# Performance work log

Hardware: AMD Instinct MI355X
Metric: run time of the kernel (lower is better)

Reference implementation:

```python
import jax, jax.numpy as jnp
import numpy as np

B, L, D = 8, 4096, 256
G, K = 64, 16
N = G * K  # 1024 slots


def _gelu(x):
    return jax.nn.gelu(x, approximate=False)  # torch nn.GELU default = exact erf


def setup_inputs() -> dict:
    key = jax.random.key(0)
    ks = jax.random.split(key, 12)
    r = lambda k, shp, s: jax.random.normal(k, shp, jnp.float32) * s
    d = D
    return {
        "X": r(ks[0], (B, L, d), 1.0),
        "S": r(ks[1], (B, N, d), 1.0),
        # projections stored (in, out); torch Linear is x @ W.T + b
        "Wgroup": r(ks[2], (d, G), d ** -0.5),
        "Wslot": r(ks[3], (d, K), d ** -0.5),
        "Wm1": r(ks[4], (d, 2 * d), d ** -0.5), "bm1": jnp.zeros((2 * d,), jnp.float32),
        "Wm2": r(ks[5], (2 * d, d), (2 * d) ** -0.5), "bm2": jnp.zeros((d,), jnp.float32),
        "Wg1": r(ks[6], (d, d), d ** -0.5), "bg1": jnp.zeros((d,), jnp.float32),
        "Wg2": r(ks[7], (d, 1), d ** -0.5), "bg2": jnp.zeros((1,), jnp.float32),
        "Wu1": r(ks[8], (2 * d, 2 * d), (2 * d) ** -0.5), "bu1": jnp.zeros((2 * d,), jnp.float32),
        "Wu2": r(ks[9], (2 * d, d), (2 * d) ** -0.5), "bu2": jnp.zeros((d,), jnp.float32),
        "ln_w": jnp.ones((d,), jnp.float32), "ln_b": jnp.zeros((d,), jnp.float32),
    }


def reference(X, S, Wgroup, Wslot, Wm1, bm1, Wm2, bm2, Wg1, bg1, Wg2, bg2,
              Wu1, bu1, Wu2, bu2, ln_w, ln_b):
    # message + gate per token
    msg = _gelu(X @ Wm1 + bm1) @ Wm2 + bm2                  # (B,L,D)
    gate = jax.nn.sigmoid(_gelu(X @ Wg1 + bg1) @ Wg2 + bg2)  # (B,L,1)
    gated_msg = msg * gate                                   # (B,L,D)

    # eval-mode hierarchical WTA: hard argmax one-hot routing (group, then slot)
    group_idx = jnp.argmax(X @ Wgroup, axis=-1)              # (B,L) in [0,G)
    slot_idx = jnp.argmax(X @ Wslot, axis=-1)                # (B,L) in [0,K)
    flat_slot = group_idx * K + slot_idx                     # (B,L) in [0,N)

    # one-hot bmm == scatter-sum of gated messages into slots (exact same math)
    seg = (flat_slot + jnp.arange(B)[:, None] * N).reshape(-1)  # (B*L,)
    incoming = jax.ops.segment_sum(gated_msg.reshape(B * L, D), seg,
                                   num_segments=B * N).reshape(B, N, D)

    # slot update + LayerNorm
    h = jnp.concatenate([S, incoming], axis=-1)              # (B,N,2D)
    S_new = S + (_gelu(h @ Wu1 + bu1) @ Wu2 + bu2)
    mu = S_new.mean(-1, keepdims=True)
    var = S_new.var(-1, keepdims=True)
    return (S_new - mu) * jax.lax.rsqrt(var + 1e-5) * ln_w + ln_b
```

## Files before the change

### kernel.cpp

```cpp
#include <hip/hip_runtime.h>
#include <hip/hip_bf16.h>

using bf16 = __hip_bfloat16;
typedef __attribute__((ext_vector_type(8))) __bf16 bf16x8;
typedef __attribute__((ext_vector_type(4))) float f32x4;

namespace {

constexpr int D     = 256;
constexpr int NTOK  = 32768;
constexpr int NSLOT = 8192;
constexpr int GG    = 64;
constexpr int KK    = 16;
constexpr int NN    = 1024;

__device__ __forceinline__ float erf_fast(float x){
  const float ax = fabsf(x);
  const float tt = 1.0f / fmaf(0.3275911f, ax, 1.0f);
  float p = fmaf(1.061405429f, tt, -1.453152027f);
  p = fmaf(p, tt, 1.421413741f);
  p = fmaf(p, tt, -0.284496736f);
  p = fmaf(p, tt, 0.254829592f);
  p *= tt;
  const float e = __expf(-ax*ax);
  const float r = 1.0f - p*e;
  return copysignf(r, x);
}

__device__ __forceinline__ float gelu_f(float x){
  return 0.5f * x * (1.0f + erf_fast(x * 0.70710678118654752f));
}

struct alignas(16) ushort8s { unsigned short v[8]; };

__device__ __forceinline__ ushort8s pack8(const float* src){
  const float4 f0 = reinterpret_cast<const float4*>(src)[0];
  const float4 f1 = reinterpret_cast<const float4*>(src)[1];
  ushort8s u;
  u.v[0] = __bfloat16_as_ushort(__float2bfloat16(f0.x));
  u.v[1] = __bfloat16_as_ushort(__float2bfloat16(f0.y));
  u.v[2] = __bfloat16_as_ushort(__float2bfloat16(f0.z));
  u.v[3] = __bfloat16_as_ushort(__float2bfloat16(f0.w));
  u.v[4] = __bfloat16_as_ushort(__float2bfloat16(f1.x));
  u.v[5] = __bfloat16_as_ushort(__float2bfloat16(f1.y));
  u.v[6] = __bfloat16_as_ushort(__float2bfloat16(f1.z));
  u.v[7] = __bfloat16_as_ushort(__float2bfloat16(f1.w));
  return u;
}


__global__ void prep_w_k(const float* __restrict__ Wm1, const float* __restrict__ Wg1,
                         const float* __restrict__ Wm2, const float* __restrict__ Wu1,
                         const float* __restrict__ Wu2, const float* __restrict__ Wgr,
                         const float* __restrict__ Wsl, const float* __restrict__ bm1,
                         const float* __restrict__ bg1,
                         bf16* __restrict__ W1p, bf16* __restrict__ W2p,
                         bf16* __restrict__ Wu1p, bf16* __restrict__ Wu2p,
                         float* __restrict__ Wcat, float* __restrict__ bcat)
{
  const int idx = blockIdx.x*256 + threadIdx.x;
  if (idx < 196608){
    const int e = idx&7, q = (idx>>3)&3, f = (idx>>5)&15, tile = idx>>9;
    const int kt = tile&7, ng = tile>>3;
    const int n = ng*16+f, k = kt*32+q*8+e;
    W1p[idx] = __float2bfloat16(n < 512 ? Wm1[k*512+n] : Wg1[k*256+(n-512)]);
  } else if (idx < 327680){
    const int i = idx-196608;
    const int e = i&7, q = (i>>3)&3, f = (i>>5)&15, tile = i>>9;
    const int kt = tile&15, ng = tile>>4;
    W2p[i] = __float2bfloat16(Wm2[(kt*32+q*8+e)*256 + ng*16+f]);
  } else if (idx < 589824){
    const int i = idx-327680;
    const int e = i&7, q = (i>>3)&3, f = (i>>5)&15, tile = i>>9;
    const int kt = tile&15, ng = tile>>4;
    Wu1p[i] = __float2bfloat16(Wu1[(kt*32+q*8+e)*512 + ng*16+f]);
  } else if (idx < 720896){
    const int i = idx-589824;
    const int e = i&7, q = (i>>3)&3, f = (i>>5)&15, tile = i>>9;
    const int kt = tile&15, ng = tile>>4;
    Wu2p[i] = __float2bfloat16(Wu2[(kt*32+q*8+e)*256 + ng*16+f]);
  } else if (idx < 741376){
    const int i = idx - 720896, k = i / 80, c = i - k*80;
    Wcat[i] = (c < GG) ? Wgr[k*GG + c] : Wsl[k*KK + (c - GG)];
  } else if (idx < 742144){
    const int c = idx - 741376;
    bcat[c] = (c < 512) ? bm1[c] : bg1[c - 512];
  }
}

__global__ void cvt_pack_x_k(const float* __restrict__ X, bf16* __restrict__ Xp){
  const int chunk = blockIdx.x*256 + threadIdx.x;
  const int q = chunk&3, f = (chunk>>2)&15, tile = chunk>>6;
  const int kt = tile&7, ng = tile>>3;
  const float* src = X + (size_t)(ng*16+f)*256 + kt*32 + q*8;
  reinterpret_cast<ushort8s*>(Xp)[chunk] = pack8(src);
}

__global__ void pack_h_k(const float* __restrict__ S, const float* __restrict__ inc,
                         bf16* __restrict__ Hp){
  const int chunk = blockIdx.x*256 + threadIdx.x;
  const int q = chunk&3, f = (chunk>>2)&15, tile = chunk>>6;
  const int kt = tile&15, ng = tile>>4;
  const int r = ng*16+f, c = kt*32+q*8;
  const float* src = (c < 256) ? (S + (size_t)r*256 + c) : (inc + (size_t)r*256 + (c-256));
  reinterpret_cast<ushort8s*>(Hp)[chunk] = pack8(src);
}

template<int K, int N1, int NG, int N2, int BM, int EPI>
__global__ __launch_bounds__(512, 2) void fused2_k(
    const bf16* __restrict__ Ap,
    const bf16* __restrict__ W1p, const float* __restrict__ b1,
    const bf16* __restrict__ W2p, const float* __restrict__ b2,
    void* __restrict__ Cout,
    const float* __restrict__ S, const float* __restrict__ lnw, const float* __restrict__ lnb,
    const float* __restrict__ Wg2,
    const int* __restrict__ slotp, const float* __restrict__ bg2p, float* __restrict__ incp)
{
  constexpr int SLICE = (N1 + NG) / 8;
  constexpr int SP    = SLICE / 32;
  constexpr int MF    = BM / 16;
  constexpr int NKA   = K / 32;
  constexpr int NKB   = N1 / 32;
  constexpr int H1B   = BM * N1 * 2;
  __shared__ alignas(16) char smem[H1B];
  __shared__ float gate_lds[EPI == 2 ? BM : 1];
  __shared__ int   slot_lds[EPI == 2 ? BM : 1];

  const int t = threadIdx.x, lane = t & 63, w = t >> 6;
  const int fRow = lane & 15, kq = lane >> 4, kOff = kq * 8;
  const int lo8 = (fRow*4 + kq) * 8;
  const int bm0 = blockIdx.x * BM;

  if constexpr (EPI == 2){
    if (t < BM){ gate_lds[t] = 0.f; slot_lds[t] = slotp[bm0 + t]; }
    __syncthreads();
  }

  f32x4 acc[MF][2];

  for (int sp = 0; sp < SP; ++sp){
    const int colb = w * SLICE + sp * 32;
    const bf16* bp0 = W1p + ((size_t)((colb>>4)    ) * NKA) * 512 + lo8;
    const bf16* bp1 = W1p + ((size_t)((colb>>4) + 1) * NKA) * 512 + lo8;

#pragma unroll
    for (int mf = 0; mf < MF; ++mf)
#pragma unroll
      for (int j = 0; j < 2; ++j)
#pragma unroll
        for (int r = 0; r < 4; ++r) acc[mf][j][r] = 0.f;

#pragma unroll
    for (int kt = 0; kt < NKA; ++kt){
      const bf16x8 b0  = *reinterpret_cast<const bf16x8*>(bp0 + kt*512);
      const bf16x8 b1v = *reinterpret_cast<const bf16x8*>(bp1 + kt*512);
#pragma unroll
      for (int mf = 0; mf < MF; ++mf){
        const bf16x8 a = *reinterpret_cast<const bf16x8*>(
            Ap + ((size_t)((bm0>>4) + mf) * NKA + kt) * 512 + lo8);
        acc[mf][0] = __builtin_amdgcn_mfma_f32_16x16x32_bf16(a, b0,  acc[mf][0], 0, 0, 0);
        acc[mf][1] = __builtin_amdgcn_mfma_f32_16x16x32_bf16(a, b1v, acc[mf][1], 0, 0, 0);
      }
    }

    if (NG == 0 || colb < N1){
#pragma unroll
      for (int mf = 0; mf < MF; ++mf){
#pragma unroll
        for (int j = 0; j < 2; ++j){
          const int col = colb + j*16 + fRow;
          const float bvx = b1[col];
#pragma unroll
          for (int r = 0; r < 4; ++r){
            const int row = mf*16 + kq*4 + r;
            const float v = gelu_f(acc[mf][j][r] + bvx);
            const unsigned off = ((unsigned)(row*N1 + col)*2u) ^ ((unsigned)(row & 7) << 4);
            *(bf16*)(smem + off) = __float2bfloat16(v);
          }
        }
      }
    } else if constexpr (NG > 0 && EPI == 2){
      const float b1v0 = b1[colb + fRow],       b1v1 = b1[colb + 16 + fRow];
      const float wg0  = Wg2[colb - N1 + fRow], wg1  = Wg2[colb - N1 + 16 + fRow];
#pragma unroll
      for (int mf = 0; mf < MF; ++mf){
#pragma unroll
        for (int r = 0; r < 4; ++r){
          float p = gelu_f(acc[mf][0][r] + b1v0) * wg0
                  + gelu_f(acc[mf][1][r] + b1v1) * wg1;
          p += __shfl_xor(p, 1); p += __shfl_xor(p, 2);
          p += __shfl_xor(p, 4); p += __shfl_xor(p, 8);
          if (fRow == 0) atomicAdd(&gate_lds[mf*16 + kq*4 + r], p);
        }
      }
    }
  }
  __syncthreads();

  if constexpr (EPI == 2){
    if (t < BM) gate_lds[t] = 1.f / (1.f + __expf(-(gate_lds[t] + bg2p[0])));
  }

  const int colb2 = w * (N2 / 8);
  const bf16* cp0 = W2p + ((size_t)((colb2>>4)    ) * NKB) * 512 + lo8;
  const bf16* cp1 = W2p + ((size_t)((colb2>>4) + 1) * NKB) * 512 + lo8;

#pragma unroll
  for (int mf = 0; mf < MF; ++mf)
#pragma unroll
    for (int j = 0; j < 2; ++j)
#pragma unroll
      for (int r = 0; r < 4; ++r) acc[mf][j][r] = 0.f;

#pragma unroll
  for (int kt = 0; kt < NKB; ++kt){
    const bf16x8 c0 = *reinterpret_cast<const bf16x8*>(cp0 + kt*512);
    const bf16x8 c1 = *reinterpret_cast<const bf16x8*>(cp1 + kt*512);
#pragma unroll
    for (int mf = 0; mf < MF; ++mf){
      const int row = mf*16 + fRow;
      const unsigned off = ((unsigned)(row*N1 + kt*32 + kOff)*2u) ^ ((unsigned)(row & 7) << 4);
      const bf16x8 af = *reinterpret_cast<const bf16x8*>(smem + off);
      acc[mf][0] = __builtin_amdgcn_mfma_f32_16x16x32_bf16(af, c0, acc[mf][0], 0, 0, 0);
      acc[mf][1] = __builtin_amdgcn_mfma_f32_16x16x32_bf16(af, c1, acc[mf][1], 0, 0, 0);
    }
  }

  if constexpr (EPI == 2){
    __syncthreads();
    const int bb = bm0 >> 12;
#pragma unroll
    for (int mf = 0; mf < MF; ++mf){
      float gr[4]; int sl[4];
#pragma unroll
      for (int r = 0; r < 4; ++r){
        const int row = mf*16 + kq*4 + r;
        gr[r] = gate_lds[row];
        sl[r] = slot_lds[row];
      }
#pragma unroll
      for (int j = 0; j < 2; ++j){
        const int col = colb2 + j*16 + fRow;
        const float bvx = b2[col];
#pragma unroll
        for (int r = 0; r < 4; ++r)
          atomicAdd(incp + ((size_t)(bb*NN + sl[r]))*D + col, (acc[mf][j][r] + bvx) * gr[r]);
      }
    }
  } else {
    float vals[MF][2][4];
#pragma unroll
    for (int mf = 0; mf < MF; ++mf){
      const int row0 = mf*16 + kq*4;
#pragma unroll
      for (int j = 0; j < 2; ++j){
        const int col = colb2 + j*16 + fRow;
        const float bvx = b2[col];
#pragma unroll
        for (int r = 0; r < 4; ++r)
          vals[mf][j][r] = S[(size_t)(bm0 + row0 + r)*N2 + col] + acc[mf][j][r] + bvx;
      }
    }
    __syncthreads();
    float* red = (float*)smem;
#pragma unroll
    for (int mf = 0; mf < MF; ++mf)
#pragma unroll
      for (int r = 0; r < 4; ++r){
        float s = 0.f, q = 0.f;
#pragma unroll
        for (int j = 0; j < 2; ++j){ s += vals[mf][j][r]; q += vals[mf][j][r]*vals[mf][j][r]; }
        s += __shfl_xor(s, 1); s += __shfl_xor(s, 2); s += __shfl_xor(s, 4); s += __shfl_xor(s, 8);
        q += __shfl_xor(q, 1); q += __shfl_xor(q, 2); q += __shfl_xor(q, 4); q += __shfl_xor(q, 8);
        if (fRow == 0){
          const int row = mf*16 + kq*4 + r;
          red[(row*8 + w)*2 + 0] = s;
          red[(row*8 + w)*2 + 1] = q;
        }
      }
    __syncthreads();
    float* mur = (float*)smem + BM*8*2;
    if (t < BM){
      float s = 0.f, q = 0.f;
      for (int w2 = 0; w2 < 8; w2++){ s += red[(t*8 + w2)*2]; q += red[(t*8 + w2)*2 + 1]; }
      const float mu = s * (1.f/256.f);
      const float var = q * (1.f/256.f) - mu*mu;
      mur[t*2] = mu; mur[t*2 + 1] = rsqrtf(var + 1e-5f);
    }
    __syncthreads();
#pragma unroll
    for (int mf = 0; mf < MF; ++mf){
      const int row0 = mf*16 + kq*4;
#pragma unroll
      for (int j = 0; j < 2; ++j){
        const int col = colb2 + j*16 + fRow;
        const float lw = lnw[col], lb = lnb[col];
#pragma unroll
        for (int r = 0; r < 4; ++r){
          const int row = row0 + r;
          ((float*)Cout)[(size_t)(bm0 + row)*N2 + col] =
              (vals[mf][j][r] - mur[row*2]) * mur[row*2 + 1] * lw + lb;
        }
      }
    }
  }
}

__global__ __launch_bounds__(256) void route4_k(const float* __restrict__ X,
                                                const float* __restrict__ Wcat,
                                                int* __restrict__ slot_out)
{
  __shared__ float lds[128 * 84];
  float* Xs = lds;
  float* Ws = lds + 16 * 136;
  float* Cs = lds;

  const int t = threadIdx.x;
  const int tok0 = blockIdx.x * 128;
  const int cq = t & 15;
  const int tg = t >> 4;
  const int stok = t >> 2, skq = t & 3;

  const float* xsrc0 = X + (size_t)(tok0 + stok) * D + 4*skq;
  const float* xsrc1 = X + (size_t)(tok0 + 64 + stok) * D + 4*skq;
  const int wrow0 = t / 20,        wc0 = t - wrow0*20;
  const int wrow1 = (256+t) / 20,  wc1 = (256+t) - wrow1*20;

  float accg[8][4] = {};
  float accs[8] = {};

  float4 xr0 = *reinterpret_cast<const float4*>(xsrc0);
  float4 xr1 = *reinterpret_cast<const float4*>(xsrc1);
  float4 wr0 = *reinterpret_cast<const float4*>(Wcat + (size_t)wrow0*80 + 4*wc0);
  float4 wr1;
  if (t < 64) wr1 = *reinterpret_cast<const float4*>(Wcat + (size_t)wrow1*80 + 4*wc1);

  for (int kt = 0; kt < 16; ++kt){
    __syncthreads();
    Xs[(4*skq+0)*136 + stok] = xr0.x;
    Xs[(4*skq+1)*136 + stok] = xr0.y;
    Xs[(4*skq+2)*136 + stok] = xr0.z;
    Xs[(4*skq+3)*136 + stok] = xr0.w;
    Xs[(4*skq+0)*136 + 64 + stok] = xr1.x;
    Xs[(4*skq+1)*136 + 64 + stok] = xr1.y;
    Xs[(4*skq+2)*136 + 64 + stok] = xr1.z;
    Xs[(4*skq+3)*136 + 64 + stok] = xr1.w;
    *reinterpret_cast<float4*>(&Ws[wrow0*80 + 4*wc0]) = wr0;
    if (t < 64) *reinterpret_cast<float4*>(&Ws[wrow1*80 + 4*wc1]) = wr1;
    __syncthreads();
    if (kt < 15){
      const int ko = (kt+1)*16;
      xr0 = *reinterpret_cast<const float4*>(xsrc0 + ko);
      xr1 = *reinterpret_cast<const float4*>(xsrc1 + ko);
      wr0 = *reinterpret_cast<const float4*>(Wcat + (size_t)(ko + wrow0)*80 + 4*wc0);
      if (t < 64) wr1 = *reinterpret_cast<const float4*>(Wcat + (size_t)(ko + wrow1)*80 + 4*wc1);
    }
#pragma unroll
    for (int k = 0; k < 16; ++k){
      const float4 xa = *reinterpret_cast<const float4*>(&Xs[k*136 + tg*8]);
      const float4 xb = *reinterpret_cast<const float4*>(&Xs[k*136 + tg*8 + 4]);
      const float4 wq = *reinterpret_cast<const float4*>(&Ws[k*80 + 4*cq]);
      const float wsv = Ws[k*80 + 64 + cq];
      const float xv[8] = {xa.x, xa.y, xa.z, xa.w, xb.x, xb.y, xb.z, xb.w};
#pragma unroll
      for (int m = 0; m < 8; m++){
        accg[m][0] = fmaf(xv[m], wq.x, accg[m][0]);
        accg[m][1] = fmaf(xv[m], wq.y, accg[m][1]);
        accg[m][2] = fmaf(xv[m], wq.z, accg[m][2]);
        accg[m][3] = fmaf(xv[m], wq.w, accg[m][3]);
        accs[m]    = fmaf(xv[m], wsv,  accs[m]);
      }
    }
  }

  __syncthreads();
#pragma unroll
  for (int m = 0; m < 8; m++){
    const int tok = tg*8 + m;
    Cs[tok*84 + 4*cq + 0] = accg[m][0];
    Cs[tok*84 + 4*cq + 1] = accg[m][1];
    Cs[tok*84 + 4*cq + 2] = accg[m][2];
    Cs[tok*84 + 4*cq + 3] = accg[m][3];
    Cs[tok*84 + 64 + cq]  = accs[m];
  }
  __syncthreads();
  if (t < 128){
    const float* row = &Cs[t * 84];
    float bg = row[0]; int big = 0;
    for (int g = 1; g < 64; ++g){ const float v = row[g]; if (v > bg){ bg = v; big = g; } }
    float bs = row[64]; int bis = 0;
    for (int s2 = 1; s2 < 16; ++s2){ const float v = row[64 + s2]; if (v > bs){ bs = v; bis = s2; } }
    slot_out[tok0 + t] = big * KK + bis;
  }
}

}

extern "C" void kernel_launch(void* const* d_in, const int* in_sizes, int n_in,
                              void* d_out, int out_size, void* d_ws, size_t ws_size,
                              hipStream_t stream)
{
  (void)in_sizes; (void)n_in; (void)out_size; (void)ws_size;
  const float* X   = (const float*)d_in[0];
  const float* S   = (const float*)d_in[1];
  const float* Wgr = (const float*)d_in[2];
  const float* Wsl = (const float*)d_in[3];
  const float* Wm1 = (const float*)d_in[4];
  const float* bm1 = (const float*)d_in[5];
  const float* Wm2 = (const float*)d_in[6];
  const float* bm2 = (const float*)d_in[7];
  const float* Wg1 = (const float*)d_in[8];
  const float* bg1 = (const float*)d_in[9];
  const float* Wg2 = (const float*)d_in[10];
  const float* bg2 = (const float*)d_in[11];
  const float* Wu1 = (const float*)d_in[12];
  const float* bu1 = (const float*)d_in[13];
  const float* Wu2 = (const float*)d_in[14];
  const float* bu2 = (const float*)d_in[15];
  const float* lnw = (const float*)d_in[16];
  const float* lnb = (const float*)d_in[17];
  float* out = (float*)d_out;

  char* ws = (char*)d_ws;
  bf16* Xp   = (bf16*)(ws + 0);
  bf16* Hp   = (bf16*)(ws + 16777216);
  bf16* W1p  = (bf16*)(ws + 67108864);
  bf16* W2p  = (bf16*)(ws + 67108864 + 393216);
  bf16* Wu1p = (bf16*)(ws + 67108864 + 655360);
  bf16* Wu2p = (bf16*)(ws + 67108864 + 1179648);
  int*   slot = (int*)  (ws + 68550656);
  float* inc  = (float*)(ws + 68812800);
  float* Wcat = (float*)(ws + 77201408);
  float* bcat = (float*)(ws + 77201408 + 81920);

  prep_w_k<<<(742144 + 255)/256, 256, 0, stream>>>(Wm1, Wg1, Wm2, Wu1, Wu2, Wgr, Wsl, bm1, bg1,
                                                   W1p, W2p, Wu1p, Wu2p, Wcat, bcat);
  cvt_pack_x_k<<<4096, 256, 0, stream>>>(X, Xp);

  route4_k<<<NTOK/128, 256, 0, stream>>>(X, Wcat, slot);
  hipMemsetAsync(inc, 0, (size_t)NSLOT*D*sizeof(float), stream);

  fused2_k<256, 512, 256, 256, 64, 2><<<NTOK/64, 512, 0, stream>>>(
      Xp, W1p, bcat, W2p, bm2, nullptr,
      nullptr, nullptr, nullptr, Wg2, slot, bg2, inc);

  pack_h_k<<<2048, 256, 0, stream>>>(S, inc, Hp);

  fused2_k<512, 512, 0, 256, 32, 1><<<NSLOT/32, 512, 0, stream>>>(
      Hp, Wu1p, bu1, Wu2p, bu2, out,
      S, lnw, lnb, nullptr, nullptr, nullptr, nullptr);
}
```

Before: 161.2 us.

## Fuse routing argmax into the message/gate fused kernel prologue

Removes the separate route4_k kernel and computes the group/slot projection plus argmax inside the EPI==2 fused2_k kernel prologue, using LDS for the X and Wcat tiles. This drops one kernel launch and the round trip of slot indices through global memory. In exchange, each 64-token block now does the fp32 routing GEMM without register prefetching, using a less register-blocked scheme of 2 tokens per thread and extra barriers. That may add latency ahead of the main MFMA work.

Result: slower. 173.7 us (+7.8%).

```diff
diff --git a/kernel.cpp b/kernel.cpp
--- a/kernel.cpp
+++ b/kernel.cpp
@@ -114,7 +114,8 @@
     void* __restrict__ Cout,
     const float* __restrict__ S, const float* __restrict__ lnw, const float* __restrict__ lnb,
     const float* __restrict__ Wg2,
-    const int* __restrict__ slotp, const float* __restrict__ bg2p, float* __restrict__ incp)
+    const float* __restrict__ Xf, const float* __restrict__ Wcat,
+    const float* __restrict__ bg2p, float* __restrict__ incp)
 {
   constexpr int SLICE = (N1 + NG) / 8;
   constexpr int SP    = SLICE / 32;
@@ -131,12 +132,66 @@
   const int lo8 = (fRow*4 + kq) * 8;
   const int bm0 = blockIdx.x * BM;
 
+  f32x4 acc[MF][2];
+
   if constexpr (EPI == 2){
-    if (t < BM){ gate_lds[t] = 0.f; slot_lds[t] = slotp[bm0 + t]; }
-    __syncthreads();
-  }
-
-  f32x4 acc[MF][2];
+    float* Xc = (float*)smem;
+    float* Wc = (float*)(smem + 4352);
+    const int cq = t & 15, tg = t >> 4;
+    float ag0[4] = {0.f,0.f,0.f,0.f}, ag1[4] = {0.f,0.f,0.f,0.f};
+    float as0 = 0.f, as1 = 0.f;
+    for (int kt16 = 0; kt16 < 16; ++kt16){
+      __syncthreads();
+      if (t < 256){
+        const int tok = t >> 2, q4 = (t & 3) * 4;
+        const float4 xv = *reinterpret_cast<const float4*>(
+            Xf + (size_t)(bm0 + tok)*256 + kt16*16 + q4);
+        Xc[(q4+0)*68 + tok] = xv.x;
+        Xc[(q4+1)*68 + tok] = xv.y;
+        Xc[(q4+2)*68 + tok] = xv.z;
+        Xc[(q4+3)*68 + tok] = xv.w;
+      } else {
+        const int c2 = t - 256;
+#pragma unroll
+        for (int j = 0; j < 5; ++j){
+          const int flat = c2*5 + j;
+          Wc[flat] = Wcat[kt16*1280 + flat];
+        }
+      }
+      __syncthreads();
+#pragma unroll
+      for (int k = 0; k < 16; ++k){
+        const float x0 = Xc[k*68 + tg*2], x1 = Xc[k*68 + tg*2 + 1];
+        const float4 wq = *reinterpret_cast<const float4*>(&Wc[k*80 + 4*cq]);
+        const float wsv = Wc[k*80 + 64 + cq];
+        ag0[0] = fmaf(x0, wq.x, ag0[0]); ag0[1] = fmaf(x0, wq.y, ag0[1]);
+        ag0[2] = fmaf(x0, wq.z, ag0[2]); ag0[3] = fmaf(x0, wq.w, ag0[3]);
+        ag1[0] = fmaf(x1, wq.x, ag1[0]); ag1[1] = fmaf(x1, wq.y, ag1[1]);
+        ag1[2] = fmaf(x1, wq.z, ag1[2]); ag1[3] = fmaf(x1, wq.w, ag1[3]);
+        as0 = fmaf(x0, wsv, as0); as1 = fmaf(x1, wsv, as1);
+      }
+    }
+    __syncthreads();
+    float* Cs = (float*)smem;
+#pragma unroll
+    for (int j = 0; j < 4; ++j){
+      Cs[(tg*2+0)*84 + 4*cq + j] = ag0[j];
+      Cs[(tg*2+1)*84 + 4*cq + j] = ag1[j];
+    }
+    Cs[(tg*2+0)*84 + 64 + cq] = as0;
+    Cs[(tg*2+1)*84 + 64 + cq] = as1;
+    __syncthreads();
+    if (t < BM){
+      const float* row = &Cs[t*84];
+      float bg = row[0]; int big = 0;
+      for (int g = 1; g < 64; ++g){ const float v = row[g]; if (v > bg){ bg = v; big = g; } }
+      float bs = row[64]; int bis = 0;
+      for (int s2 = 1; s2 < 16; ++s2){ const float v = row[64+s2]; if (v > bs){ bs = v; bis = s2; } }
+      slot_lds[t] = big * KK + bis;
+      gate_lds[t] = 0.f;
+    }
+    __syncthreads();
+  }
 
   for (int sp = 0; sp < SP; ++sp){
     const int colb = w * SLICE + sp * 32;
@@ -303,94 +358,6 @@
         }
       }
     }
-  }
-}
-
-__global__ __launch_bounds__(256) void route4_k(const float* __restrict__ X,
-                                                const float* __restrict__ Wcat,
-                                                int* __restrict__ slot_out)
-{
-  __shared__ float lds[128 * 84];
-  float* Xs = lds;
-  float* Ws = lds + 16 * 136;
-  float* Cs = lds;
-
-  const int t = threadIdx.x;
-  const int tok0 = blockIdx.x * 128;
-  const int cq = t & 15;
-  const int tg = t >> 4;
-  const int stok = t >> 2, skq = t & 3;
-
-  const float* xsrc0 = X + (size_t)(tok0 + stok) * D + 4*skq;
-  const float* xsrc1 = X + (size_t)(tok0 + 64 + stok) * D + 4*skq;
-  const int wrow0 = t / 20,        wc0 = t - wrow0*20;
-  const int wrow1 = (256+t) / 20,  wc1 = (256+t) - wrow1*20;
-
-  float accg[8][4] = {};
-  float accs[8] = {};
-
-  float4 xr0 = *reinterpret_cast<const float4*>(xsrc0);
-  float4 xr1 = *reinterpret_cast<const float4*>(xsrc1);
-  float4 wr0 = *reinterpret_cast<const float4*>(Wcat + (size_t)wrow0*80 + 4*wc0);
-  float4 wr1;
-  if (t < 64) wr1 = *reinterpret_cast<const float4*>(Wcat + (size_t)wrow1*80 + 4*wc1);
-
-  for (int kt = 0; kt < 16; ++kt){
-    __syncthreads();
-    Xs[(4*skq+0)*136 + stok] = xr0.x;
-    Xs[(4*skq+1)*136 + stok] = xr0.y;
-    Xs[(4*skq+2)*136 + stok] = xr0.z;
-    Xs[(4*skq+3)*136 + stok] = xr0.w;
-    Xs[(4*skq+0)*136 + 64 + stok] = xr1.x;
-    Xs[(4*skq+1)*136 + 64 + stok] = xr1.y;
-    Xs[(4*skq+2)*136 + 64 + stok] = xr1.z;
-    Xs[(4*skq+3)*136 + 64 + stok] = xr1.w;
-    *reinterpret_cast<float4*>(&Ws[wrow0*80 + 4*wc0]) = wr0;
-    if (t < 64) *reinterpret_cast<float4*>(&Ws[wrow1*80 + 4*wc1]) = wr1;
-    __syncthreads();
-    if (kt < 15){
-      const int ko = (kt+1)*16;
-      xr0 = *reinterpret_cast<const float4*>(xsrc0 + ko);
-      xr1 = *reinterpret_cast<const float4*>(xsrc1 + ko);
-      wr0 = *reinterpret_cast<const float4*>(Wcat + (size_t)(ko + wrow0)*80 + 4*wc0);
-      if (t < 64) wr1 = *reinterpret_cast<const float4*>(Wcat + (size_t)(ko + wrow1)*80 + 4*wc1);
-    }
-#pragma unroll
-    for (int k = 0; k < 16; ++k){
-      const float4 xa = *reinterpret_cast<const float4*>(&Xs[k*136 + tg*8]);
-      const float4 xb = *reinterpret_cast<const float4*>(&Xs[k*136 + tg*8 + 4]);
-      const float4 wq = *reinterpret_cast<const float4*>(&Ws[k*80 + 4*cq]);
-      const float wsv = Ws[k*80 + 64 + cq];
-      const float xv[8] = {xa.x, xa.y, xa.z, xa.w, xb.x, xb.y, xb.z, xb.w};
-#pragma unroll
-      for (int m = 0; m < 8; m++){
-        accg[m][0] = fmaf(xv[m], wq.x, accg[m][0]);
-        accg[m][1] = fmaf(xv[m], wq.y, accg[m][1]);
-        accg[m][2] = fmaf(xv[m], wq.z, accg[m][2]);
-        accg[m][3] = fmaf(xv[m], wq.w, accg[m][3]);
-        accs[m]    = fmaf(xv[m], wsv,  accs[m]);
-      }
-    }
-  }
-
-  __syncthreads();
-#pragma unroll
-  for (int m = 0; m < 8; m++){
-    const int tok = tg*8 + m;
-    Cs[tok*84 + 4*cq + 0] = accg[m][0];
-    Cs[tok*84 + 4*cq + 1] = accg[m][1];
-    Cs[tok*84 + 4*cq + 2] = accg[m][2];
-    Cs[tok*84 + 4*cq + 3] = accg[m][3];
-    Cs[tok*84 + 64 + cq]  = accs[m];
-  }
-  __syncthreads();
-  if (t < 128){
-    const float* row = &Cs[t * 84];
-    float bg = row[0]; int big = 0;
-    for (int g = 1; g < 64; ++g){ const float v = row[g]; if (v > bg){ bg = v; big = g; } }
-    float bs = row[64]; int bis = 0;
-    for (int s2 = 1; s2 < 16; ++s2){ const float v = row[64 + s2]; if (v > bs){ bs = v; bis = s2; } }
-    slot_out[tok0 + t] = big * KK + bis;
   }
 }
 
@@ -428,7 +395,6 @@
   bf16* W2p  = (bf16*)(ws + 67108864 + 393216);
   bf16* Wu1p = (bf16*)(ws + 67108864 + 655360);
   bf16* Wu2p = (bf16*)(ws + 67108864 + 1179648);
-  int*   slot = (int*)  (ws + 68550656);
   float* inc  = (float*)(ws + 68812800);
   float* Wcat = (float*)(ws + 77201408);
   float* bcat = (float*)(ws + 77201408 + 81920);
@@ -436,17 +402,15 @@
   prep_w_k<<<(742144 + 255)/256, 256, 0, stream>>>(Wm1, Wg1, Wm2, Wu1, Wu2, Wgr, Wsl, bm1, bg1,
                                                    W1p, W2p, Wu1p, Wu2p, Wcat, bcat);
   cvt_pack_x_k<<<4096, 256, 0, stream>>>(X, Xp);
-
-  route4_k<<<NTOK/128, 256, 0, stream>>>(X, Wcat, slot);
   hipMemsetAsync(inc, 0, (size_t)NSLOT*D*sizeof(float), stream);
 
   fused2_k<256, 512, 256, 256, 64, 2><<<NTOK/64, 512, 0, stream>>>(
       Xp, W1p, bcat, W2p, bm2, nullptr,
-      nullptr, nullptr, nullptr, Wg2, slot, bg2, inc);
+      nullptr, nullptr, nullptr, Wg2, X, Wcat, bg2, inc);
 
   pack_h_k<<<2048, 256, 0, stream>>>(S, inc, Hp);
 
   fused2_k<512, 512, 0, 256, 32, 1><<<NSLOT/32, 512, 0, stream>>>(
       Hp, Wu1p, bu1, Wu2p, bu2, out,
-      S, lnw, lnb, nullptr, nullptr, nullptr, nullptr);
-}
+      S, lnw, lnb, nullptr, nullptr, nullptr, nullptr, nullptr);
+}
```
